# Kernel tuning notes

Measured on AMD Instinct MI355X. Metric: run time of the kernel, lower is better.

Reference implementation:

```python
import jax, jax.numpy as jnp
import numpy as np

N = 131072   # total nodes in batch
E = 524288   # directed edges
B = 2048     # number of graphs
H = 128      # hidden_dim
NF = 30      # node_feature_dim
GF = 4415    # gene_feature_dim
L = 3        # gnn_layers
EPS = 1e-5   # batchnorm eps


def setup_inputs() -> dict:
    key = jax.random.key(0)
    ks = jax.random.split(key, 24)
    rn = lambda k, s, sc=0.05: jax.random.normal(k, s, jnp.float32) * sc
    return {
        "x": jax.random.normal(ks[0], (N, NF), jnp.float32),
        "gene_features": jax.random.normal(ks[1], (B, GF), jnp.float32),
        "edge_index": jax.random.randint(ks[2], (2, E), 0, N),
        "batch": (jnp.arange(N) * B) // N,  # sorted, every graph non-empty
        "W_emb": rn(ks[3], (NF, H)), "b_emb": jnp.zeros((H,), jnp.float32),
        "Wg": rn(ks[4], (L, H, H)), "bg": jnp.zeros((L, H), jnp.float32),
        "bn_gamma": jnp.ones((L, H), jnp.float32), "bn_beta": jnp.zeros((L, H), jnp.float32),
        "Wd1": rn(ks[5], (2 * H, H)), "bd1": jnp.zeros((H,), jnp.float32),
        "Wd2": rn(ks[6], (H, H)), "bd2": jnp.zeros((H,), jnp.float32),
        "Wge1": rn(ks[7], (GF, 256)), "bge1": jnp.zeros((256,), jnp.float32),
        "g_gamma": jnp.ones((256,), jnp.float32), "g_beta": jnp.zeros((256,), jnp.float32),
        "Wge2": rn(ks[8], (256, H)), "bge2": jnp.zeros((H,), jnp.float32),
        "Wh1": rn(ks[9], (2 * H, H)), "bh1": jnp.zeros((H,), jnp.float32),
        "h_gamma": jnp.ones((H,), jnp.float32), "h_beta": jnp.zeros((H,), jnp.float32),
        "Wh2": rn(ks[10], (H, 64)), "bh2": jnp.zeros((64,), jnp.float32),
        "Wh3": rn(ks[11], (64, 1)), "bh3": jnp.zeros((1,), jnp.float32),
    }


def _bn_eval(x, gamma, beta):
    # inference batchnorm with running_mean=0, running_var=1
    return x * (gamma / jnp.sqrt(1.0 + EPS)) + beta


def _gcn_conv(h, W, b, src, dst):
    # PyG GCNConv: add self-loops, symmetric deg normalization, W first, bias after agg
    hw = h @ W                                            # [N,H]
    loop = jnp.arange(N)
    src_a = jnp.concatenate([src, loop])                  # [E+N]
    dst_a = jnp.concatenate([dst, loop])
    deg = jax.ops.segment_sum(jnp.ones((E + N,), hw.dtype), dst_a, num_segments=N)
    dinv = jnp.where(deg > 0, jax.lax.rsqrt(deg), 0.0)
    norm = dinv[src_a] * dinv[dst_a]                      # [E+N]
    msgs = hw[src_a] * norm[:, None]                      # gather [E+N,H]
    out = jax.ops.segment_sum(msgs, dst_a, num_segments=N)
    return out + b


def reference(x, gene_features, edge_index, batch, W_emb, b_emb, Wg, bg, bn_gamma,
              bn_beta, Wd1, bd1, Wd2, bd2, Wge1, bge1, g_gamma, g_beta, Wge2, bge2,
              Wh1, bh1, h_gamma, h_beta, Wh2, bh2, Wh3, bh3):
    src, dst = edge_index[0], edge_index[1]
    h = jax.nn.relu(x @ W_emb + b_emb)                    # [N,H]
    for i in range(L):
        hn = _gcn_conv(h, Wg[i], bg[i], src, dst)
        hn = jax.nn.relu(_bn_eval(hn, bn_gamma[i], bn_beta[i]))
        h = hn if i == 0 else h + hn                      # residual for i>0
    # global mean / max pooling per graph
    counts = jax.ops.segment_sum(jnp.ones((N,), h.dtype), batch, num_segments=B)
    mean_pool = jax.ops.segment_sum(h, batch, num_segments=B) / jnp.maximum(counts, 1.0)[:, None]
    max_pool = jax.ops.segment_max(h, batch, num_segments=B)
    graph_repr = jnp.concatenate([mean_pool, max_pool], axis=1)   # [B,2H]
    drug = jax.nn.relu(graph_repr @ Wd1 + bd1) @ Wd2 + bd2        # [B,H]
    g1 = jax.nn.relu(_bn_eval(gene_features @ Wge1 + bge1, g_gamma, g_beta))
    gene = jax.nn.relu(g1 @ Wge2 + bge2)                          # [B,H]
    comb = jnp.concatenate([drug, gene], axis=1)                  # [B,2H]
    z = jax.nn.relu(_bn_eval(comb @ Wh1 + bh1, h_gamma, h_beta))
    z = jax.nn.relu(z @ Wh2 + bh2)
    return z @ Wh3 + bh3                                          # [B,1]
```

## Files before the change

### kernel.cpp

```cpp
#include <hip/hip_runtime.h>

#define N_NODES 131072
#define E_EDGES 524288
#define B_GR    2048
#define H_DIM   128
#define NF_DIM  30
#define GF_DIM  4415
#define GF_PAD  4416
#define BN_SCALE 0.9999950000374997f

typedef __bf16 bf16x8 __attribute__((ext_vector_type(8)));
typedef float  f32x4  __attribute__((ext_vector_type(4)));
typedef unsigned int uint32;
typedef uint32 u32x4 __attribute__((ext_vector_type(4)));

__device__ __forceinline__ void split2(float x, __bf16& hi, __bf16& lo){
    hi = (__bf16)x;
    lo = (__bf16)(x - (float)hi);
}
__device__ __forceinline__ uint32 bfbits(float x){
    __bf16 h = (__bf16)x;
    return (uint32)__builtin_bit_cast(unsigned short, h);
}
__device__ __forceinline__ float unpack_even(uint32 u){ return __uint_as_float(u<<16); }
__device__ __forceinline__ float unpack_odd (uint32 u){ return __uint_as_float(u & 0xffff0000u); }
__device__ __forceinline__ uint32 pack2(float e, float o){ return bfbits(e) | (bfbits(o)<<16); }


__global__ void k_zero_int(int* __restrict__ p, int n){
    int i = blockIdx.x*256 + threadIdx.x;
    if(i < n) p[i] = 0;
}

__global__ void k_count(const int* __restrict__ dst, int* __restrict__ counts){
    int e = blockIdx.x*256 + threadIdx.x;
    if(e < E_EDGES) atomicAdd(&counts[dst[e]], 1);
}

__global__ void k_scan1(int* __restrict__ counts, int* __restrict__ bsums){
    __shared__ int s[1024];
    int t = threadIdx.x;
    int gi = blockIdx.x*1024 + t;
    int v = counts[gi];
    s[t] = v; __syncthreads();
    for(int off=1; off<1024; off<<=1){
        int x = (t>=off) ? s[t-off] : 0;
        __syncthreads();
        s[t] += x;
        __syncthreads();
    }
    counts[gi] = s[t] - v;
    if(t == 1023) bsums[blockIdx.x] = s[t];
}

__global__ void k_scan2(int* __restrict__ bsums){
    __shared__ int s[128];
    int t = threadIdx.x;
    int v = bsums[t]; s[t] = v; __syncthreads();
    for(int off=1; off<128; off<<=1){
        int x = (t>=off) ? s[t-off] : 0;
        __syncthreads();
        s[t] += x;
        __syncthreads();
    }
    bsums[t] = s[t] - v;
}

__global__ void k_scan3(const int* __restrict__ counts, const int* __restrict__ bsums,
                        int* __restrict__ rowptr){
    int i = blockIdx.x*1024 + threadIdx.x;
    rowptr[i] = counts[i] + bsums[blockIdx.x];
    if(i == 0) rowptr[N_NODES] = E_EDGES;
}

__global__ void k_dinv_cursor(const int* __restrict__ rowptr, float* __restrict__ dinv,
                              int* __restrict__ cursor){
    int n = blockIdx.x*256 + threadIdx.x;
    if(n < N_NODES){
        int a = rowptr[n], b = rowptr[n+1];
        dinv[n] = rsqrtf((float)(b - a) + 1.0f);
        cursor[n] = a;
    }
}

__global__ void k_fill(const int* __restrict__ src, const int* __restrict__ dst,
                       int* __restrict__ cursor, int* __restrict__ csr){
    int e = blockIdx.x*256 + threadIdx.x;
    if(e < E_EDGES){
        int p = atomicAdd(&cursor[dst[e]], 1);
        csr[p] = src[e];
    }
}


__global__ void k_split_x(const float* __restrict__ x, __bf16* __restrict__ xh,
                          __bf16* __restrict__ xl){
    int idx = blockIdx.x*256 + threadIdx.x;
    int n = idx >> 5, k = idx & 31;
    float v = (k < NF_DIM) ? x[n*NF_DIM + k] : 0.f;
    split2(v, xh[idx], xl[idx]);
}

__global__ void k_split_wemb(const float* __restrict__ W, __bf16* __restrict__ th,
                             __bf16* __restrict__ tl){
    int idx = blockIdx.x*256 + threadIdx.x;
    int c = idx >> 5, k = idx & 31;
    float v = (k < NF_DIM) ? W[k*H_DIM + c] : 0.f;
    split2(v, th[idx], tl[idx]);
}

__global__ void k_split_wg(const float* __restrict__ Wg, __bf16* __restrict__ th,
                           __bf16* __restrict__ tl){
    int idx = blockIdx.x*256 + threadIdx.x;
    int l = idx >> 14, i = idx & 16383;
    int k = i >> 7, c = i & 127;
    float v = Wg[idx];
    int o = (l << 14) + (c << 7) + k;
    split2(v, th[o], tl[o]);
}

__global__ void k_split_gf(const float* __restrict__ gf, __bf16* __restrict__ ah,
                           __bf16* __restrict__ al){
    unsigned idx = blockIdx.x*256 + threadIdx.x;
    unsigned r = idx / GF_PAD, k = idx - r*GF_PAD;
    float v = (k < GF_DIM) ? gf[(size_t)r*GF_DIM + k] : 0.f;
    split2(v, ah[idx], al[idx]);
}

__global__ void k_split_wge1(const float* __restrict__ W, __bf16* __restrict__ th,
                             __bf16* __restrict__ tl){
    unsigned idx = blockIdx.x*256 + threadIdx.x;
    unsigned c = idx / GF_PAD, k = idx - c*GF_PAD;
    float v = (k < GF_DIM) ? W[(size_t)k*256 + c] : 0.f;
    split2(v, th[idx], tl[idx]);
}


__global__ __launch_bounds__(256)
void k_emb_mfma(const __bf16* __restrict__ xh, const __bf16* __restrict__ xl,
                const __bf16* __restrict__ wth, const __bf16* __restrict__ wtl,
                const float* __restrict__ bias, uint32* __restrict__ Hh2,
                uint32* __restrict__ Hl2){
    __shared__ float sT[4][32*68];
    int wave = threadIdx.x >> 6, lane = threadIdx.x & 63;
    int lr = lane & 15, lq = lane >> 4;
    int rbase = blockIdx.x*128 + wave*32;
    const f32x4 zero4 = {0.f,0.f,0.f,0.f};
    bf16x8 A0h = *(const bf16x8*)(xh + (size_t)(rbase + lr)*32 + lq*8);
    bf16x8 A0l = *(const bf16x8*)(xl + (size_t)(rbase + lr)*32 + lq*8);
    bf16x8 A1h = *(const bf16x8*)(xh + (size_t)(rbase + 16 + lr)*32 + lq*8);
    bf16x8 A1l = *(const bf16x8*)(xl + (size_t)(rbase + 16 + lr)*32 + lq*8);
    int orow = lane >> 3;
    int oq   = lane & 7;
    float* sW = sT[wave];
    for(int ph=0; ph<2; ph++){
        #pragma unroll
        for(int cc=0; cc<4; cc++){
            int col = (ph*4+cc)*16 + lr;
            bf16x8 Bh = *(const bf16x8*)(wth + col*32 + lq*8);
            bf16x8 Bl = *(const bf16x8*)(wtl + col*32 + lq*8);
            f32x4 a0 = zero4, a1 = zero4;
            a0 = __builtin_amdgcn_mfma_f32_16x16x32_bf16(A0h, Bh, a0, 0,0,0);
            a0 = __builtin_amdgcn_mfma_f32_16x16x32_bf16(A0l, Bh, a0, 0,0,0);
            a0 = __builtin_amdgcn_mfma_f32_16x16x32_bf16(A0h, Bl, a0, 0,0,0);
            a1 = __builtin_amdgcn_mfma_f32_16x16x32_bf16(A1h, Bh, a1, 0,0,0);
            a1 = __builtin_amdgcn_mfma_f32_16x16x32_bf16(A1l, Bh, a1, 0,0,0);
            a1 = __builtin_amdgcn_mfma_f32_16x16x32_bf16(A1h, Bl, a1, 0,0,0);
            #pragma unroll
            for(int r=0;r<4;r++){
                sW[(lq*4+r)*68 + cc*16 + lr]    = a0[r];
                sW[(16+lq*4+r)*68 + cc*16 + lr] = a1[r];
            }
        }
        __syncthreads();
        int cg = ph*64 + oq*8;
        float bb[8];
        *(float4*)&bb[0] = *(const float4*)(bias + cg);
        *(float4*)&bb[4] = *(const float4*)(bias + cg + 4);
        #pragma unroll
        for(int i=0;i<4;i++){
            int row = i*8 + orow;
            float v[8];
            *(float4*)&v[0] = *(float4*)&sW[row*68 + oq*8];
            *(float4*)&v[4] = *(float4*)&sW[row*68 + oq*8 + 4];
            uint32 oh[4], ol[4];
            #pragma unroll
            for(int p=0;p<4;p++){
                float ve = fmaxf(v[2*p]   + bb[2*p],   0.f);
                float vo = fmaxf(v[2*p+1] + bb[2*p+1], 0.f);
                uint32 he = bfbits(ve), ho = bfbits(vo);
                oh[p] = he | (ho<<16);
                float le = ve - __uint_as_float(he<<16);
                float lo = vo - __uint_as_float(ho<<16);
                ol[p] = pack2(le, lo);
            }
            size_t oidx = (size_t)(rbase + row)*64 + (cg>>1);
            *(uint4*)(Hh2 + oidx) = make_uint4(oh[0],oh[1],oh[2],oh[3]);
            *(uint4*)(Hl2 + oidx) = make_uint4(ol[0],ol[1],ol[2],ol[3]);
        }
        __syncthreads();
    }
}


struct AggMeta {
    int   j0A, cA, j0B, cB;
    float dnA, dnB;
    uint32 shA, slA, shB, slB;
    int   jjA[8], jjB[8];
};

__device__ __forceinline__ void agg_load_meta(AggMeta& m, int nA, int lane,
                                              const int* __restrict__ rowptr,
                                              const float* __restrict__ dinv,
                                              const uint32* __restrict__ Hh2,
                                              const uint32* __restrict__ Hl2){
    int nB = nA + 8;
    int a0 = rowptr[nA], a1 = rowptr[nA+1];
    int b0 = rowptr[nB], b1 = rowptr[nB+1];
    m.j0A = a0; m.cA = a1 - a0;
    m.j0B = b0; m.cB = b1 - b0;
    m.dnA = dinv[nA]; m.dnB = dinv[nB];
    size_t iA = (size_t)nA*64 + lane, iB = (size_t)nB*64 + lane;
    m.shA = Hh2[iA]; m.slA = Hl2[iA];
    m.shB = Hh2[iB]; m.slB = Hl2[iB];
}

__device__ __forceinline__ void agg_load_csr(AggMeta& m, const int* __restrict__ csr){
    int jmA = m.j0A + m.cA - 1;
    int jmB = m.j0B + m.cB - 1;
    #pragma unroll
    for(int t=0;t<8;t++){
        int ia = m.j0A + t; ia = ia > jmA ? jmA : ia;
        int ib = m.j0B + t; ib = ib > jmB ? jmB : ib;
        m.jjA[t] = csr[ia] & (N_NODES-1);
        m.jjB[t] = csr[ib] & (N_NODES-1);
    }
}

__device__ __forceinline__ void agg_pair(AggMeta& cur, AggMeta& nxt, int ii, bool pf,
                                         int rbase, int base16, int lane,
                                         const uint32* __restrict__ Hh2,
                                         const uint32* __restrict__ Hl2,
                                         const float* __restrict__ dinv,
                                         const int* __restrict__ rowptr,
                                         const int* __restrict__ csr,
                                         uint32* __restrict__ AhL,
                                         uint32* __restrict__ AlL){
    uint32 rrA[8], rrB[8];
    float  wwA[8], wwB[8];
    #pragma unroll
    for(int t=0;t<8;t++){
        wwA[t] = (t < cur.cA) ? dinv[cur.jjA[t]] : 0.f;
        rrA[t] = Hh2[(size_t)cur.jjA[t]*64 + lane];
        wwB[t] = (t < cur.cB) ? dinv[cur.jjB[t]] : 0.f;
        rrB[t] = Hh2[(size_t)cur.jjB[t]*64 + lane];
    }
    if(pf){
        agg_load_meta(nxt, rbase + base16 + ii + 1, lane, rowptr, dinv, Hh2, Hl2);
        agg_load_csr(nxt, csr);
    }
    float axA = (unpack_even(cur.shA) + unpack_even(cur.slA)) * cur.dnA;
    float ayA = (unpack_odd(cur.shA)  + unpack_odd(cur.slA))  * cur.dnA;
    float axB = (unpack_even(cur.shB) + unpack_even(cur.slB)) * cur.dnB;
    float ayB = (unpack_odd(cur.shB)  + unpack_odd(cur.slB))  * cur.dnB;
    #pragma unroll
    for(int t=0;t<8;t++){
        axA = fmaf(unpack_even(rrA[t]), wwA[t], axA);
        ayA = fmaf(unpack_odd(rrA[t]),  wwA[t], ayA);
        axB = fmaf(unpack_even(rrB[t]), wwB[t], axB);
        ayB = fmaf(unpack_odd(rrB[t]),  wwB[t], ayB);
    }
    int nb = cur.cA > cur.cB ? cur.cA : cur.cB;
    if(nb > 8){
        int jmA = cur.j0A + cur.cA - 1;
        int jmB = cur.j0B + cur.cB - 1;
        for(int j=8; j<nb; j+=8){
            int jja[8], jjb[8]; float wa[8], wb[8]; uint32 ra[8], rb[8];
            #pragma unroll
            for(int t=0;t<8;t++){
                int ia = cur.j0A + j + t; ia = ia > jmA ? jmA : ia;
                int ib = cur.j0B + j + t; ib = ib > jmB ? jmB : ib;
                jja[t] = csr[ia] & (N_NODES-1);
                jjb[t] = csr[ib] & (N_NODES-1);
            }
            #pragma unroll
            for(int t=0;t<8;t++){
                wa[t] = (j + t < cur.cA) ? dinv[jja[t]] : 0.f;
                ra[t] = Hh2[(size_t)jja[t]*64 + lane];
                wb[t] = (j + t < cur.cB) ? dinv[jjb[t]] : 0.f;
                rb[t] = Hh2[(size_t)jjb[t]*64 + lane];
            }
            #pragma unroll
            for(int t=0;t<8;t++){
                axA = fmaf(unpack_even(ra[t]), wa[t], axA);
                ayA = fmaf(unpack_odd(ra[t]),  wa[t], ayA);
                axB = fmaf(unpack_even(rb[t]), wb[t], axB);
                ayB = fmaf(unpack_odd(rb[t]),  wb[t], ayB);
            }
        }
    }
    axA *= cur.dnA; ayA *= cur.dnA;
    axB *= cur.dnB; ayB *= cur.dnB;
    int rowA = base16 + ii, rowB = rowA + 8;
    uint32 hxA = bfbits(axA), hyA = bfbits(ayA);
    AhL[rowA*68 + lane] = hxA | (hyA<<16);
    AlL[rowA*68 + lane] = pack2(axA - __uint_as_float(hxA<<16),
                                ayA - __uint_as_float(hyA<<16));
    uint32 hxB = bfbits(axB), hyB = bfbits(ayB);
    AhL[rowB*68 + lane] = hxB | (hyB<<16);
    AlL[rowB*68 + lane] = pack2(axB - __uint_as_float(hxB<<16),
                                ayB - __uint_as_float(hyB<<16));
}

__global__ __launch_bounds__(512, 4)
void k_layer(const __bf16* __restrict__ curHh, const __bf16* __restrict__ curHl,
             const float* __restrict__ dinv, const int* __restrict__ rowptr,
             const int* __restrict__ csr,
             const __bf16* __restrict__ Bth, const __bf16* __restrict__ Btl,
             const float* __restrict__ bias, const float* __restrict__ gamma,
             const float* __restrict__ beta,
             uint32* __restrict__ outHh2, uint32* __restrict__ outHl2, int residual){
    __shared__ uint32 smem[8*32*68];
    uint32* AhL = smem;
    uint32* AlL = smem + 128*68;
    int tid  = threadIdx.x;
    int wave = __builtin_amdgcn_readfirstlane(tid >> 6);
    int lane = tid & 63;
    int rbase = blockIdx.x * 128;
    int base16 = wave*16;
    const uint32* Hh2 = (const uint32*)curHh;
    const uint32* Hl2 = (const uint32*)curHl;

    {
        AggMeta m0, m1;
        agg_load_meta(m0, rbase + base16 + 0, lane, rowptr, dinv, Hh2, Hl2);
        agg_load_csr(m0, csr);
        agg_pair(m0, m1, 0, true,  rbase, base16, lane, Hh2, Hl2, dinv, rowptr, csr, AhL, AlL);
        agg_pair(m1, m0, 1, true,  rbase, base16, lane, Hh2, Hl2, dinv, rowptr, csr, AhL, AlL);
        agg_pair(m0, m1, 2, true,  rbase, base16, lane, Hh2, Hl2, dinv, rowptr, csr, AhL, AlL);
        agg_pair(m1, m0, 3, true,  rbase, base16, lane, Hh2, Hl2, dinv, rowptr, csr, AhL, AlL);
        agg_pair(m0, m1, 4, true,  rbase, base16, lane, Hh2, Hl2, dinv, rowptr, csr, AhL, AlL);
        agg_pair(m1, m0, 5, true,  rbase, base16, lane, Hh2, Hl2, dinv, rowptr, csr, AhL, AlL);
        agg_pair(m0, m1, 6, true,  rbase, base16, lane, Hh2, Hl2, dinv, rowptr, csr, AhL, AlL);
        agg_pair(m1, m0, 7, false, rbase, base16, lane, Hh2, Hl2, dinv, rowptr, csr, AhL, AlL);
    }
    __syncthreads();

    int lr = lane & 15, lq = lane >> 4;
    int wr = wave & 3, wc = wave >> 2;
    int r0 = wr*32;
    bf16x8 A0h[4], A0l[4], A1h[4], A1l[4];
    #pragma unroll
    for(int ks=0;ks<4;ks++){
        int u0 = (r0 + lr)*68 + lq*4 + ks*16;
        int u1 = (r0 + 16 + lr)*68 + lq*4 + ks*16;
        A0h[ks] = __builtin_bit_cast(bf16x8, *(const u32x4*)(AhL + u0));
        A0l[ks] = __builtin_bit_cast(bf16x8, *(const u32x4*)(AlL + u0));
        A1h[ks] = __builtin_bit_cast(bf16x8, *(const u32x4*)(AhL + u1));
        A1l[ks] = __builtin_bit_cast(bf16x8, *(const u32x4*)(AlL + u1));
    }
    __syncthreads();

    float* stg = (float*)smem + wave*(32*68);
    const f32x4 zero4 = {0.f,0.f,0.f,0.f};
    #pragma unroll
    for(int cc=0; cc<4; cc++){
        int col = wc*64 + cc*16 + lr;
        f32x4 a0 = zero4, a1 = zero4;
        #pragma unroll
        for(int ks=0;ks<4;ks++){
            bf16x8 Bh = *(const bf16x8*)(Bth + col*H_DIM + ks*32 + lq*8);
            bf16x8 Bl = *(const bf16x8*)(Btl + col*H_DIM + ks*32 + lq*8);
            a0 = __builtin_amdgcn_mfma_f32_16x16x32_bf16(A0h[ks], Bh, a0, 0,0,0);
            a0 = __builtin_amdgcn_mfma_f32_16x16x32_bf16(A0l[ks], Bh, a0, 0,0,0);
            a0 = __builtin_amdgcn_mfma_f32_16x16x32_bf16(A0h[ks], Bl, a0, 0,0,0);
            a1 = __builtin_amdgcn_mfma_f32_16x16x32_bf16(A1h[ks], Bh, a1, 0,0,0);
            a1 = __builtin_amdgcn_mfma_f32_16x16x32_bf16(A1l[ks], Bh, a1, 0,0,0);
            a1 = __builtin_amdgcn_mfma_f32_16x16x32_bf16(A1h[ks], Bl, a1, 0,0,0);
        }
        #pragma unroll
        for(int r=0;r<4;r++){
            stg[(lq*4+r)*68 + cc*16 + lr]    = a0[r];
            stg[(16+lq*4+r)*68 + cc*16 + lr] = a1[r];
        }
    }

    int orow = lane >> 3;
    int oq   = lane & 7;
    int cg = wc*64 + oq*8;
    float bb[8], gg[8], tt[8];
    *(float4*)&bb[0] = *(const float4*)(bias + cg);
    *(float4*)&bb[4] = *(const float4*)(bias + cg + 4);
    *(float4*)&gg[0] = *(const float4*)(gamma + cg);
    *(float4*)&gg[4] = *(const float4*)(gamma + cg + 4);
    *(float4*)&tt[0] = *(const float4*)(beta + cg);
    *(float4*)&tt[4] = *(const float4*)(beta + cg + 4);
    #pragma unroll
    for(int p=0;p<8;p++) gg[p] *= BN_SCALE;
    #pragma unroll
    for(int i=0;i<4;i++){
        int row = i*8 + orow;
        float v[8];
        *(float4*)&v[0] = *(float4*)&stg[row*68 + oq*8];
        *(float4*)&v[4] = *(float4*)&stg[row*68 + oq*8 + 4];
        size_t oidx = (size_t)(rbase + r0 + row)*64 + (cg>>1);
        uint4 oldh = {0,0,0,0}, oldl = {0,0,0,0};
        if(residual){
            oldh = *(const uint4*)(Hh2 + oidx);
            oldl = *(const uint4*)(Hl2 + oidx);
        }
        uint32 ohv[4] = {oldh.x,oldh.y,oldh.z,oldh.w};
        uint32 olv[4] = {oldl.x,oldl.y,oldl.z,oldl.w};
        uint32 oh[4], ol[4];
        #pragma unroll
        for(int p=0;p<4;p++){
            float ve = fmaxf(fmaf(v[2*p]   + bb[2*p],   gg[2*p],   tt[2*p]),   0.f);
            float vo = fmaxf(fmaf(v[2*p+1] + bb[2*p+1], gg[2*p+1], tt[2*p+1]), 0.f);
            if(residual){
                ve += unpack_even(ohv[p]) + unpack_even(olv[p]);
                vo += unpack_odd(ohv[p])  + unpack_odd(olv[p]);
            }
            uint32 he = bfbits(ve), ho = bfbits(vo);
            oh[p] = he | (ho<<16);
            float le = ve - __uint_as_float(he<<16);
            float lo = vo - __uint_as_float(ho<<16);
            ol[p] = pack2(le, lo);
        }
        *(uint4*)(outHh2 + oidx) = make_uint4(oh[0],oh[1],oh[2],oh[3]);
        *(uint4*)(outHl2 + oidx) = make_uint4(ol[0],ol[1],ol[2],ol[3]);
    }
}


__global__ __launch_bounds__(256)
void k_gemm_gf_mfma(const __bf16* __restrict__ Ah, const __bf16* __restrict__ Al,
                    const __bf16* __restrict__ Bth, const __bf16* __restrict__ Btl,
                    float* __restrict__ gpart){
    int rt = blockIdx.x & 31;
    int sp = blockIdx.x >> 5;
    int ks0 = (sp*138) >> 3, ks1 = ((sp+1)*138) >> 3;
    int wave = threadIdx.x >> 6, lane = threadIdx.x & 63;
    int lr = lane & 15, lq = lane >> 4;
    int rbase = rt*64 + (wave & 1)*32;
    int cbase = (wave >> 1)*128;
    const f32x4 zero4 = {0.f,0.f,0.f,0.f};
    f32x4 acc[8][2];
    #pragma unroll
    for(int ct=0;ct<8;ct++){ acc[ct][0] = zero4; acc[ct][1] = zero4; }
    for(int ks=ks0; ks<ks1; ks++){
        int kc = ks*32;
        size_t oa0 = (size_t)(rbase + lr)*GF_PAD + kc + lq*8;
        size_t oa1 = oa0 + (size_t)16*GF_PAD;
        bf16x8 A0h = *(const bf16x8*)(Ah + oa0);
        bf16x8 A0l = *(const bf16x8*)(Al + oa0);
        bf16x8 A1h = *(const bf16x8*)(Ah + oa1);
        bf16x8 A1l = *(const bf16x8*)(Al + oa1);
        #pragma unroll
        for(int ct=0;ct<8;ct++){
            size_t bo = (size_t)(cbase + ct*16 + lr)*GF_PAD + kc + lq*8;
            bf16x8 Bh = *(const bf16x8*)(Bth + bo);
            bf16x8 Bl = *(const bf16x8*)(Btl + bo);
            acc[ct][0] = __builtin_amdgcn_mfma_f32_16x16x32_bf16(A0h, Bh, acc[ct][0], 0,0,0);
            acc[ct][0] = __builtin_amdgcn_mfma_f32_16x16x32_bf16(A0l, Bh, acc[ct][0], 0,0,0);
            acc[ct][0] = __builtin_amdgcn_mfma_f32_16x16x32_bf16(A0h, Bl, acc[ct][0], 0,0,0);
            acc[ct][1] = __builtin_amdgcn_mfma_f32_16x16x32_bf16(A1h, Bh, acc[ct][1], 0,0,0);
            acc[ct][1] = __builtin_amdgcn_mfma_f32_16x16x32_bf16(A1l, Bh, acc[ct][1], 0,0,0);
            acc[ct][1] = __builtin_amdgcn_mfma_f32_16x16x32_bf16(A1h, Bl, acc[ct][1], 0,0,0);
        }
    }
    float* po = gpart + (size_t)sp*(B_GR*256);
    #pragma unroll
    for(int ct=0;ct<8;ct++)
        #pragma unroll
        for(int s=0;s<2;s++)
            #pragma unroll
            for(int r=0;r<4;r++)
                po[(size_t)(rbase + s*16 + lq*4 + r)*256 + cbase + ct*16 + lr] = acc[ct][s][r];
}

__global__ void k_gene_reduce(const float* __restrict__ gpart, const float* __restrict__ bias,
                              const float* __restrict__ gamma, const float* __restrict__ beta,
                              float* __restrict__ g1){
    int i = blockIdx.x*256 + threadIdx.x;
    int c = i & 255;
    float v = bias[c];
    #pragma unroll
    for(int sp=0;sp<8;sp++) v += gpart[(size_t)sp*(B_GR*256) + i];
    v = fmaf(v, gamma[c]*BN_SCALE, beta[c]);
    g1[i] = fmaxf(v, 0.f);
}


__global__ __launch_bounds__(256)
void k_pool(const uint32* __restrict__ Hh2, const uint32* __restrict__ Hl2,
            float* __restrict__ pool){
    __shared__ float red[4][4][64];
    int g = blockIdx.x;
    int wave = threadIdx.x >> 6, lane = threadIdx.x & 63;
    size_t base = (size_t)g*64*64 + (size_t)wave*16*64 + lane;
    float se = 0.f, so = 0.f, me = -3.4e38f, mo = -3.4e38f;
    #pragma unroll
    for(int r=0;r<16;r++){
        uint32 h = Hh2[base + r*64];
        uint32 l = Hl2[base + r*64];
        float ve = unpack_even(h) + unpack_even(l);
        float vo = unpack_odd(h)  + unpack_odd(l);
        se += ve; so += vo;
        me = fmaxf(me, ve); mo = fmaxf(mo, vo);
    }
    red[wave][0][lane] = se; red[wave][1][lane] = so;
    red[wave][2][lane] = me; red[wave][3][lane] = mo;
    __syncthreads();
    if(wave == 0){
        float s0 = red[0][0][lane] + red[1][0][lane] + red[2][0][lane] + red[3][0][lane];
        float s1 = red[0][1][lane] + red[1][1][lane] + red[2][1][lane] + red[3][1][lane];
        float m0 = fmaxf(fmaxf(red[0][2][lane], red[1][2][lane]),
                         fmaxf(red[2][2][lane], red[3][2][lane]));
        float m1 = fmaxf(fmaxf(red[0][3][lane], red[1][3][lane]),
                         fmaxf(red[2][3][lane], red[3][3][lane]));
        float2 mn = make_float2(s0*(1.f/64.f), s1*(1.f/64.f));
        float2 mx = make_float2(m0, m1);
        *(float2*)&pool[g*256 + 2*lane]       = mn;
        *(float2*)&pool[g*256 + 128 + 2*lane] = mx;
    }
}


__global__ void k_dense(const float* __restrict__ A, int ldA, const float* __restrict__ W,
                        const float* __restrict__ bias, const float* __restrict__ gamma,
                        const float* __restrict__ beta, float* __restrict__ out, int ldOut,
                        int K, int logK, int NC, int relu){
    extern __shared__ float sA[];
    int rowBase = blockIdx.x*4;
    int c = threadIdx.x;
    for(int idx=threadIdx.x; idx<4*K; idx+=NC){
        int r = idx >> logK, k = idx & (K-1);
        sA[idx] = A[(rowBase+r)*ldA + k];
    }
    __syncthreads();
    float bb = bias[c];
    float acc0=bb, acc1=bb, acc2=bb, acc3=bb;
    for(int k=0;k<K;k++){
        float w = W[k*NC + c];
        acc0 = fmaf(sA[k],     w, acc0);
        acc1 = fmaf(sA[K+k],   w, acc1);
        acc2 = fmaf(sA[2*K+k], w, acc2);
        acc3 = fmaf(sA[3*K+k], w, acc3);
    }
    float gsc = 1.f, bsh = 0.f;
    if(gamma){ gsc = gamma[c]*BN_SCALE; bsh = beta[c]; }
    float v0=acc0, v1=acc1, v2=acc2, v3=acc3;
    if(gamma){ v0=fmaf(v0,gsc,bsh); v1=fmaf(v1,gsc,bsh); v2=fmaf(v2,gsc,bsh); v3=fmaf(v3,gsc,bsh); }
    if(relu){ v0=fmaxf(v0,0.f); v1=fmaxf(v1,0.f); v2=fmaxf(v2,0.f); v3=fmaxf(v3,0.f); }
    out[(rowBase+0)*ldOut + c] = v0;
    out[(rowBase+1)*ldOut + c] = v1;
    out[(rowBase+2)*ldOut + c] = v2;
    out[(rowBase+3)*ldOut + c] = v3;
}


__global__ void k_final(const float* __restrict__ z2, const float* __restrict__ Wh3,
                        const float* __restrict__ bh3, float* __restrict__ out){
    int lane = threadIdx.x & 63, wr = threadIdx.x >> 6;
    int r = blockIdx.x*4 + wr;
    float v = z2[r*64 + lane] * Wh3[lane];
    #pragma unroll
    for(int off=32; off; off>>=1) v += __shfl_down(v, off);
    if(lane == 0) out[r] = v + bh3[0];
}


extern "C" void kernel_launch(void* const* d_in, const int* in_sizes, int n_in,
                              void* d_out, int out_size, void* d_ws, size_t ws_size,
                              hipStream_t stream){
    (void)in_sizes; (void)n_in; (void)out_size; (void)ws_size;
    const float* x    = (const float*)d_in[0];
    const float* gf   = (const float*)d_in[1];
    const int*   ei   = (const int*)  d_in[2];
    const float* W_emb= (const float*)d_in[4];
    const float* b_emb= (const float*)d_in[5];
    const float* Wg   = (const float*)d_in[6];
    const float* bg   = (const float*)d_in[7];
    const float* bn_g = (const float*)d_in[8];
    const float* bn_b = (const float*)d_in[9];
    const float* Wd1  = (const float*)d_in[10];
    const float* bd1  = (const float*)d_in[11];
    const float* Wd2  = (const float*)d_in[12];
    const float* bd2  = (const float*)d_in[13];
    const float* Wge1 = (const float*)d_in[14];
    const float* bge1 = (const float*)d_in[15];
    const float* g_g  = (const float*)d_in[16];
    const float* g_b  = (const float*)d_in[17];
    const float* Wge2 = (const float*)d_in[18];
    const float* bge2 = (const float*)d_in[19];
    const float* Wh1  = (const float*)d_in[20];
    const float* bh1  = (const float*)d_in[21];
    const float* h_g  = (const float*)d_in[22];
    const float* h_b  = (const float*)d_in[23];
    const float* Wh2  = (const float*)d_in[24];
    const float* bh2  = (const float*)d_in[25];
    const float* Wh3  = (const float*)d_in[26];
    const float* bh3  = (const float*)d_in[27];
    float* outp = (float*)d_out;

    char* base = (char*)d_ws;
    __bf16* Hh = (__bf16*)base;
    __bf16* Hl = (__bf16*)(base + (32u<<20));
    char*   R  = base + (64u<<20);
    __bf16* gfh    = (__bf16*)R;
    __bf16* gfl    = (__bf16*)(R + 18087936);
    float*  gpart  = (float*) (R + 36175872);
    __bf16* wge_th = (__bf16*)(R + 52953088);
    __bf16* wge_tl = (__bf16*)(R + 55214080);
    __bf16* xsh = (__bf16*)R;
    __bf16* xsl = (__bf16*)(R + (8u<<20));
    __bf16* Ph = (__bf16*)R;
    __bf16* Pl = (__bf16*)(R + (32u<<20));
    char* T = base + (128u<<20);
    float* pool = (float*)T;
    float* g1   = pool + B_GR*256;
    float* t1   = g1   + B_GR*256;
    float* comb = t1   + B_GR*128;
    float* z    = comb + B_GR*256;
    float* z2   = z    + B_GR*128;
    int* rowptr = (int*)(z2 + B_GR*64);
    int* cursor = rowptr + (N_NODES+1);
    int* csr    = cursor + N_NODES;
    int* bsums  = csr + E_EDGES;
    float* dinv = (float*)(bsums + 128);
    __bf16* wg_th = (__bf16*)(dinv + N_NODES);
    __bf16* wg_tl = wg_th + 3*16384;
    __bf16* we_th = wg_tl + 3*16384;
    __bf16* we_tl = we_th + 128*32;

    const int* src = ei;
    const int* dst = ei + E_EDGES;

    k_zero_int   <<<N_NODES/256, 256, 0, stream>>>(cursor, N_NODES);
    k_count      <<<E_EDGES/256, 256, 0, stream>>>(dst, cursor);
    k_scan1      <<<128, 1024, 0, stream>>>(cursor, bsums);
    k_scan2      <<<1, 128, 0, stream>>>(bsums);
    k_scan3      <<<128, 1024, 0, stream>>>(cursor, bsums, rowptr);
    k_dinv_cursor<<<N_NODES/256, 256, 0, stream>>>(rowptr, dinv, cursor);
    k_fill       <<<E_EDGES/256, 256, 0, stream>>>(src, dst, cursor, csr);

    k_split_gf    <<<(B_GR*GF_PAD)/256, 256, 0, stream>>>(gf, gfh, gfl);
    k_split_wge1  <<<(256*GF_PAD)/256, 256, 0, stream>>>(Wge1, wge_th, wge_tl);
    k_gemm_gf_mfma<<<256, 256, 0, stream>>>(gfh, gfl, wge_th, wge_tl, gpart);
    k_gene_reduce <<<(B_GR*256)/256, 256, 0, stream>>>(gpart, bge1, g_g, g_b, g1);

    k_split_x    <<<(N_NODES*32)/256, 256, 0, stream>>>(x, xsh, xsl);
    k_split_wemb <<<(128*32)/256, 256, 0, stream>>>(W_emb, we_th, we_tl);
    k_split_wg   <<<(3*16384)/256, 256, 0, stream>>>(Wg, wg_th, wg_tl);
    k_emb_mfma   <<<N_NODES/128, 256, 0, stream>>>(xsh, xsl, we_th, we_tl, b_emb,
                                                   (uint32*)Hh, (uint32*)Hl);

    {
        uint32 *curh = (uint32*)Hh, *curl = (uint32*)Hl;
        uint32 *outh = (uint32*)Ph, *outl = (uint32*)Pl;
        for(int i=0;i<3;i++){
            k_layer<<<N_NODES/128, 512, 0, stream>>>((const __bf16*)curh, (const __bf16*)curl,
                                                     dinv, rowptr, csr,
                                                     wg_th + i*16384, wg_tl + i*16384,
                                                     bg + i*H_DIM, bn_g + i*H_DIM, bn_b + i*H_DIM,
                                                     outh, outl, i > 0);
            uint32* th = curh; curh = outh; outh = th;
            uint32* tl = curl; curl = outl; outl = tl;
        }
        k_pool<<<B_GR, 256, 0, stream>>>(curh, curl, pool);
    }

    k_dense<<<B_GR/4, 128, 4*256*4, stream>>>(pool, 256, Wd1, bd1, nullptr, nullptr, t1,   128, 256, 8, 128, 1);
    k_dense<<<B_GR/4, 128, 4*128*4, stream>>>(t1,   128, Wd2, bd2, nullptr, nullptr, comb, 256, 128, 7, 128, 0);
    k_dense<<<B_GR/4, 128, 4*256*4, stream>>>(g1,   256, Wge2, bge2, nullptr, nullptr, comb+128, 256, 256, 8, 128, 1);
    k_dense<<<B_GR/4, 128, 4*256*4, stream>>>(comb, 256, Wh1, bh1, h_g, h_b, z, 128, 256, 8, 128, 1);
    k_dense<<<B_GR/4, 64,  4*128*4, stream>>>(z,    128, Wh2, bh2, nullptr, nullptr, z2, 64, 128, 7, 64, 1);
    k_final<<<B_GR/4, 256, 0, stream>>>(z2, Wh3, bh3, outp);
}
```

Before: 613.1 us.

## Fuse fp32 split into GEMM loads, merge weight splits, fuse pooling and MLP head

The separate kernels that split x and gene_features into bf16 hi/lo copies are removed. The embedding and gene GEMMs now read fp32 directly and split in registers, which avoids writing and re-reading the large padded bf16 gene matrix. The three weight-split kernels become one launch. Pooling and the six dense/final kernels are fused into one head kernel that handles two graphs per block. Costs: uncoalesced strided fp32 loads in the GEMMs (rows of 4415 floats, not 16B aligned) and redundant split arithmetic per tile.

```diff
diff --git a/kernel.cpp b/kernel.cpp
--- a/kernel.cpp
+++ b/kernel.cpp
@@ -93,51 +93,36 @@
 }
 
 
-__global__ void k_split_x(const float* __restrict__ x, __bf16* __restrict__ xh,
-                          __bf16* __restrict__ xl){
-    int idx = blockIdx.x*256 + threadIdx.x;
-    int n = idx >> 5, k = idx & 31;
-    float v = (k < NF_DIM) ? x[n*NF_DIM + k] : 0.f;
-    split2(v, xh[idx], xl[idx]);
-}
-
-__global__ void k_split_wemb(const float* __restrict__ W, __bf16* __restrict__ th,
-                             __bf16* __restrict__ tl){
-    int idx = blockIdx.x*256 + threadIdx.x;
-    int c = idx >> 5, k = idx & 31;
-    float v = (k < NF_DIM) ? W[k*H_DIM + c] : 0.f;
-    split2(v, th[idx], tl[idx]);
-}
-
-__global__ void k_split_wg(const float* __restrict__ Wg, __bf16* __restrict__ th,
-                           __bf16* __restrict__ tl){
-    int idx = blockIdx.x*256 + threadIdx.x;
-    int l = idx >> 14, i = idx & 16383;
-    int k = i >> 7, c = i & 127;
-    float v = Wg[idx];
-    int o = (l << 14) + (c << 7) + k;
-    split2(v, th[o], tl[o]);
-}
-
-__global__ void k_split_gf(const float* __restrict__ gf, __bf16* __restrict__ ah,
-                           __bf16* __restrict__ al){
-    unsigned idx = blockIdx.x*256 + threadIdx.x;
-    unsigned r = idx / GF_PAD, k = idx - r*GF_PAD;
-    float v = (k < GF_DIM) ? gf[(size_t)r*GF_DIM + k] : 0.f;
-    split2(v, ah[idx], al[idx]);
-}
-
-__global__ void k_split_wge1(const float* __restrict__ W, __bf16* __restrict__ th,
-                             __bf16* __restrict__ tl){
-    unsigned idx = blockIdx.x*256 + threadIdx.x;
-    unsigned c = idx / GF_PAD, k = idx - c*GF_PAD;
-    float v = (k < GF_DIM) ? W[(size_t)k*256 + c] : 0.f;
-    split2(v, th[idx], tl[idx]);
+__global__ void k_split_weights(const float* __restrict__ Wge1, __bf16* __restrict__ wth,
+                                __bf16* __restrict__ wtl,
+                                const float* __restrict__ Wg, __bf16* __restrict__ gth,
+                                __bf16* __restrict__ gtl,
+                                const float* __restrict__ Wemb, __bf16* __restrict__ eth,
+                                __bf16* __restrict__ etl){
+    unsigned bid = blockIdx.x;
+    if(bid < 4416u){
+        unsigned idx = bid*256 + threadIdx.x;
+        unsigned c = idx / GF_PAD, k = idx - c*GF_PAD;
+        float v = (k < GF_DIM) ? Wge1[(size_t)k*256 + c] : 0.f;
+        split2(v, wth[idx], wtl[idx]);
+    } else if(bid < 4416u + 192u){
+        int idx = (bid - 4416u)*256 + threadIdx.x;
+        int l = idx >> 14, i = idx & 16383;
+        int k = i >> 7, c = i & 127;
+        float v = Wg[idx];
+        int o = (l << 14) + (c << 7) + k;
+        split2(v, gth[o], gtl[o]);
+    } else {
+        int idx = (bid - 4608u)*256 + threadIdx.x;
+        int c = idx >> 5, k = idx & 31;
+        float v = (k < NF_DIM) ? Wemb[k*H_DIM + c] : 0.f;
+        split2(v, eth[idx], etl[idx]);
+    }
 }
 
 
 __global__ __launch_bounds__(256)
-void k_emb_mfma(const __bf16* __restrict__ xh, const __bf16* __restrict__ xl,
+void k_emb_mfma(const float* __restrict__ x,
                 const __bf16* __restrict__ wth, const __bf16* __restrict__ wtl,
                 const float* __restrict__ bias, uint32* __restrict__ Hh2,
                 uint32* __restrict__ Hl2){
@@ -146,10 +131,18 @@
     int lr = lane & 15, lq = lane >> 4;
     int rbase = blockIdx.x*128 + wave*32;
     const f32x4 zero4 = {0.f,0.f,0.f,0.f};
-    bf16x8 A0h = *(const bf16x8*)(xh + (size_t)(rbase + lr)*32 + lq*8);
-    bf16x8 A0l = *(const bf16x8*)(xl + (size_t)(rbase + lr)*32 + lq*8);
-    bf16x8 A1h = *(const bf16x8*)(xh + (size_t)(rbase + 16 + lr)*32 + lq*8);
-    bf16x8 A1l = *(const bf16x8*)(xl + (size_t)(rbase + 16 + lr)*32 + lq*8);
+    const float* xr0 = x + (size_t)(rbase + lr)*NF_DIM;
+    const float* xr1 = x + (size_t)(rbase + 16 + lr)*NF_DIM;
+    bf16x8 A0h, A0l, A1h, A1l;
+    #pragma unroll
+    for(int t=0;t<8;t++){
+        int k = lq*8 + t;
+        float v0 = (k < NF_DIM) ? xr0[k] : 0.f;
+        float v1 = (k < NF_DIM) ? xr1[k] : 0.f;
+        __bf16 h, l;
+        split2(v0, h, l); A0h[t] = h; A0l[t] = l;
+        split2(v1, h, l); A1h[t] = h; A1l[t] = l;
+    }
     int orow = lane >> 3;
     int oq   = lane & 7;
     float* sW = sT[wave];
@@ -434,7 +427,7 @@
 
 
 __global__ __launch_bounds__(256)
-void k_gemm_gf_mfma(const __bf16* __restrict__ Ah, const __bf16* __restrict__ Al,
+void k_gemm_gf_mfma(const float* __restrict__ Agf,
                     const __bf16* __restrict__ Bth, const __bf16* __restrict__ Btl,
                     float* __restrict__ gpart){
     int rt = blockIdx.x & 31;
@@ -450,12 +443,27 @@
     for(int ct=0;ct<8;ct++){ acc[ct][0] = zero4; acc[ct][1] = zero4; }
     for(int ks=ks0; ks<ks1; ks++){
         int kc = ks*32;
-        size_t oa0 = (size_t)(rbase + lr)*GF_PAD + kc + lq*8;
-        size_t oa1 = oa0 + (size_t)16*GF_PAD;
-        bf16x8 A0h = *(const bf16x8*)(Ah + oa0);
-        bf16x8 A0l = *(const bf16x8*)(Al + oa0);
-        bf16x8 A1h = *(const bf16x8*)(Ah + oa1);
-        bf16x8 A1l = *(const bf16x8*)(Al + oa1);
+        const float* ar0 = Agf + (size_t)(rbase + lr)*GF_DIM + kc + lq*8;
+        const float* ar1 = ar0 + (size_t)16*GF_DIM;
+        bf16x8 A0h, A0l, A1h, A1l;
+        if(kc + 32 <= GF_DIM){
+            #pragma unroll
+            for(int t=0;t<8;t++){
+                __bf16 h, l;
+                split2(ar0[t], h, l); A0h[t] = h; A0l[t] = l;
+                split2(ar1[t], h, l); A1h[t] = h; A1l[t] = l;
+            }
+        } else {
+            #pragma unroll
+            for(int t=0;t<8;t++){
+                int k = kc + lq*8 + t;
+                float v0 = 0.f, v1 = 0.f;
+                if(k < GF_DIM){ v0 = ar0[t]; v1 = ar1[t]; }
+                __bf16 h, l;
+                split2(v0, h, l); A0h[t] = h; A0l[t] = l;
+                split2(v1, h, l); A1h[t] = h; A1l[t] = l;
+            }
+        }
         #pragma unroll
         for(int ct=0;ct<8;ct++){
             size_t bo = (size_t)(cbase + ct*16 + lr)*GF_PAD + kc + lq*8;
@@ -493,81 +501,112 @@
 
 
 __global__ __launch_bounds__(256)
-void k_pool(const uint32* __restrict__ Hh2, const uint32* __restrict__ Hl2,
-            float* __restrict__ pool){
+void k_head(const uint32* __restrict__ Hh2, const uint32* __restrict__ Hl2,
+            const float* __restrict__ g1,
+            const float* __restrict__ Wd1, const float* __restrict__ bd1,
+            const float* __restrict__ Wd2, const float* __restrict__ bd2,
+            const float* __restrict__ Wge2, const float* __restrict__ bge2,
+            const float* __restrict__ Wh1, const float* __restrict__ bh1,
+            const float* __restrict__ h_g, const float* __restrict__ h_b,
+            const float* __restrict__ Wh2, const float* __restrict__ bh2,
+            const float* __restrict__ Wh3, const float* __restrict__ bh3,
+            float* __restrict__ out){
+    __shared__ float sPool[2][256];
+    __shared__ float sG1[2][256];
+    __shared__ float sT1[2][128];
+    __shared__ float sComb[2][256];
+    __shared__ float sZ[2][128];
+    __shared__ float sZ2p[2][2][64];
+    __shared__ float sZ2[2][64];
     __shared__ float red[4][4][64];
-    int g = blockIdx.x;
-    int wave = threadIdx.x >> 6, lane = threadIdx.x & 63;
-    size_t base = (size_t)g*64*64 + (size_t)wave*16*64 + lane;
-    float se = 0.f, so = 0.f, me = -3.4e38f, mo = -3.4e38f;
-    #pragma unroll
-    for(int r=0;r<16;r++){
-        uint32 h = Hh2[base + r*64];
-        uint32 l = Hl2[base + r*64];
-        float ve = unpack_even(h) + unpack_even(l);
-        float vo = unpack_odd(h)  + unpack_odd(l);
-        se += ve; so += vo;
-        me = fmaxf(me, ve); mo = fmaxf(mo, vo);
-    }
-    red[wave][0][lane] = se; red[wave][1][lane] = so;
-    red[wave][2][lane] = me; red[wave][3][lane] = mo;
-    __syncthreads();
-    if(wave == 0){
-        float s0 = red[0][0][lane] + red[1][0][lane] + red[2][0][lane] + red[3][0][lane];
-        float s1 = red[0][1][lane] + red[1][1][lane] + red[2][1][lane] + red[3][1][lane];
-        float m0 = fmaxf(fmaxf(red[0][2][lane], red[1][2][lane]),
-                         fmaxf(red[2][2][lane], red[3][2][lane]));
-        float m1 = fmaxf(fmaxf(red[0][3][lane], red[1][3][lane]),
-                         fmaxf(red[2][3][lane], red[3][3][lane]));
-        float2 mn = make_float2(s0*(1.f/64.f), s1*(1.f/64.f));
-        float2 mx = make_float2(m0, m1);
-        *(float2*)&pool[g*256 + 2*lane]       = mn;
-        *(float2*)&pool[g*256 + 128 + 2*lane] = mx;
-    }
-}
-
-
-__global__ void k_dense(const float* __restrict__ A, int ldA, const float* __restrict__ W,
-                        const float* __restrict__ bias, const float* __restrict__ gamma,
-                        const float* __restrict__ beta, float* __restrict__ out, int ldOut,
-                        int K, int logK, int NC, int relu){
-    extern __shared__ float sA[];
-    int rowBase = blockIdx.x*4;
-    int c = threadIdx.x;
-    for(int idx=threadIdx.x; idx<4*K; idx+=NC){
-        int r = idx >> logK, k = idx & (K-1);
-        sA[idx] = A[(rowBase+r)*ldA + k];
-    }
-    __syncthreads();
-    float bb = bias[c];
-    float acc0=bb, acc1=bb, acc2=bb, acc3=bb;
-    for(int k=0;k<K;k++){
-        float w = W[k*NC + c];
-        acc0 = fmaf(sA[k],     w, acc0);
-        acc1 = fmaf(sA[K+k],   w, acc1);
-        acc2 = fmaf(sA[2*K+k], w, acc2);
-        acc3 = fmaf(sA[3*K+k], w, acc3);
-    }
-    float gsc = 1.f, bsh = 0.f;
-    if(gamma){ gsc = gamma[c]*BN_SCALE; bsh = beta[c]; }
-    float v0=acc0, v1=acc1, v2=acc2, v3=acc3;
-    if(gamma){ v0=fmaf(v0,gsc,bsh); v1=fmaf(v1,gsc,bsh); v2=fmaf(v2,gsc,bsh); v3=fmaf(v3,gsc,bsh); }
-    if(relu){ v0=fmaxf(v0,0.f); v1=fmaxf(v1,0.f); v2=fmaxf(v2,0.f); v3=fmaxf(v3,0.f); }
-    out[(rowBase+0)*ldOut + c] = v0;
-    out[(rowBase+1)*ldOut + c] = v1;
-    out[(rowBase+2)*ldOut + c] = v2;
-    out[(rowBase+3)*ldOut + c] = v3;
-}
-
-
-__global__ void k_final(const float* __restrict__ z2, const float* __restrict__ Wh3,
-                        const float* __restrict__ bh3, float* __restrict__ out){
-    int lane = threadIdx.x & 63, wr = threadIdx.x >> 6;
-    int r = blockIdx.x*4 + wr;
-    float v = z2[r*64 + lane] * Wh3[lane];
-    #pragma unroll
-    for(int off=32; off; off>>=1) v += __shfl_down(v, off);
-    if(lane == 0) out[r] = v + bh3[0];
+    int tid = threadIdx.x;
+    int wave = tid >> 6, lane = tid & 63;
+    int g0 = blockIdx.x*2;
+    {
+        int g = wave >> 1;
+        size_t base = (size_t)(g0+g)*64*64 + (size_t)(wave & 1)*32*64 + lane;
+        float se = 0.f, so = 0.f, me = -3.4e38f, mo = -3.4e38f;
+        #pragma unroll
+        for(int r=0;r<32;r++){
+            uint32 h = Hh2[base + r*64];
+            uint32 l = Hl2[base + r*64];
+            float ve = unpack_even(h) + unpack_even(l);
+            float vo = unpack_odd(h)  + unpack_odd(l);
+            se += ve; so += vo;
+            me = fmaxf(me, ve); mo = fmaxf(mo, vo);
+        }
+        red[wave][0][lane] = se; red[wave][1][lane] = so;
+        red[wave][2][lane] = me; red[wave][3][lane] = mo;
+    }
+    {
+        int g = tid >> 7, c = tid & 127;
+        sG1[g][c]       = g1[(size_t)(g0+g)*256 + c];
+        sG1[g][c + 128] = g1[(size_t)(g0+g)*256 + c + 128];
+    }
+    __syncthreads();
+    if(tid < 128){
+        int g = tid >> 6, l = tid & 63;
+        float s0 = red[2*g][0][l] + red[2*g+1][0][l];
+        float s1 = red[2*g][1][l] + red[2*g+1][1][l];
+        float m0 = fmaxf(red[2*g][2][l], red[2*g+1][2][l]);
+        float m1 = fmaxf(red[2*g][3][l], red[2*g+1][3][l]);
+        sPool[g][2*l]       = s0*(1.f/64.f);
+        sPool[g][2*l+1]     = s1*(1.f/64.f);
+        sPool[g][128+2*l]   = m0;
+        sPool[g][128+2*l+1] = m1;
+    }
+    __syncthreads();
+    int g = tid >> 7, c = tid & 127;
+    {
+        float acc = bd1[c];
+        #pragma unroll 4
+        for(int k=0;k<256;k++) acc = fmaf(sPool[g][k], Wd1[k*128 + c], acc);
+        sT1[g][c] = fmaxf(acc, 0.f);
+    }
+    __syncthreads();
+    {
+        float acc = bd2[c];
+        #pragma unroll 4
+        for(int k=0;k<128;k++) acc = fmaf(sT1[g][k], Wd2[k*128 + c], acc);
+        sComb[g][c] = acc;
+        float acc2 = bge2[c];
+        #pragma unroll 4
+        for(int k=0;k<256;k++) acc2 = fmaf(sG1[g][k], Wge2[k*128 + c], acc2);
+        sComb[g][128 + c] = fmaxf(acc2, 0.f);
+    }
+    __syncthreads();
+    {
+        float acc = bh1[c];
+        #pragma unroll 4
+        for(int k=0;k<256;k++) acc = fmaf(sComb[g][k], Wh1[k*128 + c], acc);
+        acc = fmaf(acc, h_g[c]*BN_SCALE, h_b[c]);
+        sZ[g][c] = fmaxf(acc, 0.f);
+    }
+    __syncthreads();
+    {
+        int c2 = tid & 63, half = (tid >> 6) & 1;
+        float acc = 0.f;
+        #pragma unroll 4
+        for(int k=0;k<64;k++){
+            int kk = half*64 + k;
+            acc = fmaf(sZ[g][kk], Wh2[kk*64 + c2], acc);
+        }
+        sZ2p[g][half][c2] = acc;
+    }
+    __syncthreads();
+    {
+        int c2 = tid & 63, half = (tid >> 6) & 1;
+        if(half == 0)
+            sZ2[g][c2] = fmaxf(sZ2p[g][0][c2] + sZ2p[g][1][c2] + bh2[c2], 0.f);
+    }
+    __syncthreads();
+    if((wave & 1) == 0){
+        int gg = wave >> 1;
+        float v = sZ2[gg][lane] * Wh3[lane];
+        #pragma unroll
+        for(int off=32; off; off>>=1) v += __shfl_down(v, off);
+        if(lane == 0) out[g0 + gg] = v + bh3[0];
+    }
 }
 
 
@@ -607,24 +646,14 @@
     char* base = (char*)d_ws;
     __bf16* Hh = (__bf16*)base;
     __bf16* Hl = (__bf16*)(base + (32u<<20));
-    char*   R  = base + (64u<<20);
-    __bf16* gfh    = (__bf16*)R;
-    __bf16* gfl    = (__bf16*)(R + 18087936);
-    float*  gpart  = (float*) (R + 36175872);
-    __bf16* wge_th = (__bf16*)(R + 52953088);
-    __bf16* wge_tl = (__bf16*)(R + 55214080);
-    __bf16* xsh = (__bf16*)R;
-    __bf16* xsl = (__bf16*)(R + (8u<<20));
-    __bf16* Ph = (__bf16*)R;
-    __bf16* Pl = (__bf16*)(R + (32u<<20));
+    __bf16* Ph = (__bf16*)(base + (64u<<20));
+    __bf16* Pl = (__bf16*)(base + (96u<<20));
+    float*  gpart  = (float*)base;
+    __bf16* wge_th = (__bf16*)(base + (17u<<20));
+    __bf16* wge_tl = (__bf16*)(base + (17u<<20) + 2260992);
     char* T = base + (128u<<20);
-    float* pool = (float*)T;
-    float* g1   = pool + B_GR*256;
-    float* t1   = g1   + B_GR*256;
-    float* comb = t1   + B_GR*128;
-    float* z    = comb + B_GR*256;
-    float* z2   = z    + B_GR*128;
-    int* rowptr = (int*)(z2 + B_GR*64);
+    float* g1   = (float*)T;
+    int* rowptr = (int*)(g1 + B_GR*256);
     int* cursor = rowptr + (N_NODES+1);
     int* csr    = cursor + N_NODES;
     int* bsums  = csr + E_EDGES;
@@ -637,6 +666,12 @@
     const int* src = ei;
     const int* dst = ei + E_EDGES;
 
+    k_split_weights<<<4624, 256, 0, stream>>>(Wge1, wge_th, wge_tl, Wg, wg_th, wg_tl,
+                                              W_emb, we_th, we_tl);
+
+    k_gemm_gf_mfma<<<256, 256, 0, stream>>>(gf, wge_th, wge_tl, gpart);
+    k_gene_reduce <<<(B_GR*256)/256, 256, 0, stream>>>(gpart, bge1, g_g, g_b, g1);
+
     k_zero_int   <<<N_NODES/256, 256, 0, stream>>>(cursor, N_NODES);
     k_count      <<<E_EDGES/256, 256, 0, stream>>>(dst, cursor);
     k_scan1      <<<128, 1024, 0, stream>>>(cursor, bsums);
@@ -645,36 +680,22 @@
     k_dinv_cursor<<<N_NODES/256, 256, 0, stream>>>(rowptr, dinv, cursor);
     k_fill       <<<E_EDGES/256, 256, 0, stream>>>(src, dst, cursor, csr);
 
-    k_split_gf    <<<(B_GR*GF_PAD)/256, 256, 0, stream>>>(gf, gfh, gfl);
-    k_split_wge1  <<<(256*GF_PAD)/256, 256, 0, stream>>>(Wge1, wge_th, wge_tl);
-    k_gemm_gf_mfma<<<256, 256, 0, stream>>>(gfh, gfl, wge_th, wge_tl, gpart);
-    k_gene_reduce <<<(B_GR*256)/256, 256, 0, stream>>>(gpart, bge1, g_g, g_b, g1);
-
-    k_split_x    <<<(N_NODES*32)/256, 256, 0, stream>>>(x, xsh, xsl);
-    k_split_wemb <<<(128*32)/256, 256, 0, stream>>>(W_emb, we_th, we_tl);
-    k_split_wg   <<<(3*16384)/256, 256, 0, stream>>>(Wg, wg_th, wg_tl);
-    k_emb_mfma   <<<N_NODES/128, 256, 0, stream>>>(xsh, xsl, we_th, we_tl, b_emb,
-                                                   (uint32*)Hh, (uint32*)Hl);
-
-    {
-        uint32 *curh = (uint32*)Hh, *curl = (uint32*)Hl;
-        uint32 *outh = (uint32*)Ph, *outl = (uint32*)Pl;
-        for(int i=0;i<3;i++){
-            k_layer<<<N_NODES/128, 512, 0, stream>>>((const __bf16*)curh, (const __bf16*)curl,
-                                                     dinv, rowptr, csr,
-                                                     wg_th + i*16384, wg_tl + i*16384,
-                                                     bg + i*H_DIM, bn_g + i*H_DIM, bn_b + i*H_DIM,
-                                                     outh, outl, i > 0);
-            uint32* th = curh; curh = outh; outh = th;
-            uint32* tl = curl; curl = outl; outl = tl;
-        }
-        k_pool<<<B_GR, 256, 0, stream>>>(curh, curl, pool);
-    }
-
-    k_dense<<<B_GR/4, 128, 4*256*4, stream>>>(pool, 256, Wd1, bd1, nullptr, nullptr, t1,   128, 256, 8, 128, 1);
-    k_dense<<<B_GR/4, 128, 4*128*4, stream>>>(t1,   128, Wd2, bd2, nullptr, nullptr, comb, 256, 128, 7, 128, 0);
-    k_dense<<<B_GR/4, 128, 4*256*4, stream>>>(g1,   256, Wge2, bge2, nullptr, nullptr, comb+128, 256, 256, 8, 128, 1);
-    k_dense<<<B_GR/4, 128, 4*256*4, stream>>>(comb, 256, Wh1, bh1, h_g, h_b, z, 128, 256, 8, 128, 1);
-    k_dense<<<B_GR/4, 64,  4*128*4, stream>>>(z,    128, Wh2, bh2, nullptr, nullptr, z2, 64, 128, 7, 64, 1);
-    k_final<<<B_GR/4, 256, 0, stream>>>(z2, Wh3, bh3, outp);
-}
+    k_emb_mfma<<<N_NODES/128, 256, 0, stream>>>(x, we_th, we_tl, b_emb,
+                                                (uint32*)Hh, (uint32*)Hl);
+
+    uint32 *curh = (uint32*)Hh, *curl = (uint32*)Hl;
+    uint32 *outh = (uint32*)Ph, *outl = (uint32*)Pl;
+    for(int i=0;i<3;i++){
+        k_layer<<<N_NODES/128, 512, 0, stream>>>((const __bf16*)curh, (const __bf16*)curl,
+                                                 dinv, rowptr, csr,
+                                                 wg_th + i*16384, wg_tl + i*16384,
+                                                 bg + i*H_DIM, bn_g + i*H_DIM, bn_b + i*H_DIM,
+                                                 outh, outl, i > 0);
+        uint32* th = curh; curh = outh; outh = th;
+        uint32* tl = curl; curl = outl; outl = tl;
+    }
+
+    k_head<<<B_GR/2, 256, 0, stream>>>(curh, curl, g1,
+                                       Wd1, bd1, Wd2, bd2, Wge2, bge2,
+                                       Wh1, bh1, h_g, h_b, Wh2, bh2, Wh3, bh3, outp);
+}
```

New measurement: 595.8 us. 1.03x faster.
